# Optimization experiments

Measured on AMD Instinct MI355X. Metric: run time of the kernel, lower is better.

## Reference

```python
import jax, jax.numpy as jnp
import numpy as np
from jax import lax

D_MODEL = 1024
D_STATE = 16
D_CONV = 4
EXPAND = 2
HEADDIM = 64
D_INNER = EXPAND * D_MODEL            # 2048
NHEADS = D_INNER // HEADDIM           # 32
NGROUPS = 1
CONV_DIM = D_INNER + 2 * NGROUPS * D_STATE   # 2080
D_IN_PROJ = 2 * D_INNER + 2 * NGROUPS * D_STATE + NHEADS  # 4160
EPS = 1e-5


def _mamba2(x, in_proj_w, conv_w, conv_b, dt_bias, A_log, Dp, norm_w, out_proj_w):
    # x: (B, L, D_MODEL)
    Bt, L, _ = x.shape
    zxbcdt = jnp.einsum('bld,ed->ble', x, in_proj_w)  # (B,L,D_IN_PROJ)
    z, xBC, dt = jnp.split(zxbcdt, [D_INNER, D_INNER + CONV_DIM], axis=-1)
    dt = jax.nn.softplus(dt + dt_bias)               # (B,L,H)
    # depthwise causal conv over time
    xBC = jnp.swapaxes(xBC, 1, 2)                    # (B,C,L)
    xBC = lax.conv_general_dilated(
        xBC, conv_w, window_strides=(1,), padding=[(D_CONV - 1, 0)],
        feature_group_count=CONV_DIM,
        dimension_numbers=('NCH', 'OIH', 'NCH')) + conv_b[None, :, None]
    xBC = jnp.swapaxes(jax.nn.silu(xBC), 1, 2)       # (B,L,C)
    xs, Bm, Cm = jnp.split(xBC, [D_INNER, D_INNER + D_STATE], axis=-1)
    xs = xs.reshape(Bt, L, NHEADS, HEADDIM)          # (B,L,H,P)
    A = -jnp.exp(A_log)                              # (H,)
    dA = jnp.exp(dt * A)                             # (B,L,H)

    def step(h, inp):
        dA_t, dt_t, B_t, C_t, x_t = inp              # (B,H),(B,H),(B,N),(B,N),(B,H,P)
        h = h * dA_t[:, :, None, None] + jnp.einsum('bh,bn,bhp->bhpn', dt_t, B_t, x_t)
        y = jnp.einsum('bn,bhpn->bhp', C_t, h)
        return h, y

    h0 = jnp.zeros((Bt, NHEADS, HEADDIM, D_STATE), x.dtype)
    xs_seq = (jnp.swapaxes(dA, 0, 1), jnp.swapaxes(dt, 0, 1),
              jnp.swapaxes(Bm, 0, 1), jnp.swapaxes(Cm, 0, 1),
              jnp.swapaxes(xs, 0, 1))
    _, ys = lax.scan(step, h0, xs_seq)               # ys: (L,B,H,P)
    y = jnp.swapaxes(ys, 0, 1) + Dp[None, None, :, None] * xs
    y = y.reshape(Bt, L, D_INNER)
    # gated RMSNorm: gate first (norm_before_gate=False), then rmsnorm
    y = y * jax.nn.silu(z)
    y = y * lax.rsqrt(jnp.mean(y * y, axis=-1, keepdims=True) + EPS) * norm_w
    return jnp.einsum('bld,od->blo', y, out_proj_w)  # (B,L,D_MODEL)


def setup_inputs() -> dict:
    key = jax.random.key(0)
    ks = jax.random.split(key, 20)
    B, L = 2, 2048
    def mamba_params(kidx):
        k = jax.random.split(ks[kidx], 8)
        return dict(
            in_proj_w=jax.random.normal(k[0], (D_IN_PROJ, D_MODEL), jnp.float32) / np.sqrt(D_MODEL),
            conv_w=jax.random.normal(k[1], (CONV_DIM, 1, D_CONV), jnp.float32) / np.sqrt(D_CONV),
            conv_b=jax.random.normal(k[2], (CONV_DIM,), jnp.float32) * 0.01,
            dt_bias=jnp.log(jnp.expm1(jax.random.uniform(k[3], (NHEADS,), jnp.float32, 1e-3, 0.1))),
            A_log=jnp.log(jax.random.uniform(k[4], (NHEADS,), jnp.float32, 1.0, 16.0)),
            Dp=jnp.ones((NHEADS,), jnp.float32),
            norm_w=jnp.ones((D_INNER,), jnp.float32),
            out_proj_w=jax.random.normal(k[5], (D_MODEL, D_INNER), jnp.float32) / np.sqrt(D_INNER),
        )
    pf = mamba_params(1)
    pb = mamba_params(2)
    inp = {'x': jax.random.normal(ks[0], (B, L, D_MODEL), jnp.float32)}
    for name, p in (('fwd', pf), ('bwd', pb)):
        for pk, pv in p.items():
            inp[f'{name}_{pk}'] = pv
    inp['layer_out_proj_w'] = jax.random.normal(ks[3], (D_MODEL, 2 * D_MODEL), jnp.float32) / np.sqrt(2 * D_MODEL)
    inp['layer_scale'] = jnp.full((D_MODEL,), 1e-4, jnp.float32)
    return inp


def reference(x,
              fwd_in_proj_w, fwd_conv_w, fwd_conv_b, fwd_dt_bias, fwd_A_log, fwd_Dp, fwd_norm_w, fwd_out_proj_w,
              bwd_in_proj_w, bwd_conv_w, bwd_conv_b, bwd_dt_bias, bwd_A_log, bwd_Dp, bwd_norm_w, bwd_out_proj_w,
              layer_out_proj_w, layer_scale):
    h_fwd = _mamba2(x, fwd_in_proj_w, fwd_conv_w, fwd_conv_b, fwd_dt_bias, fwd_A_log, fwd_Dp, fwd_norm_w, fwd_out_proj_w)
    x_rev = jnp.flip(x, axis=1)
    h_bwd = jnp.flip(_mamba2(x_rev, bwd_in_proj_w, bwd_conv_w, bwd_conv_b, bwd_dt_bias, bwd_A_log, bwd_Dp, bwd_norm_w, bwd_out_proj_w), axis=1)
    h_bi = jnp.concatenate([h_fwd, h_bwd], axis=-1)   # (B,L,2*D_MODEL)
    mamba_out = jnp.einsum('ble,de->bld', h_bi, layer_out_proj_w)
    # dropout is identity in eval mode
    return x + mamba_out * layer_scale
```

## Files before the change

kernel.cpp:

```cpp
#include <hip/hip_runtime.h>

typedef __attribute__((ext_vector_type(8))) short bf16x8;
typedef __attribute__((ext_vector_type(4))) float f32x4;
typedef __attribute__((ext_vector_type(2))) long i64x2;

#define DEV static __device__ __forceinline__

DEV float b2f(unsigned short u) {
    union { unsigned int u; float f; } c; c.u = ((unsigned int)u) << 16; return c.f;
}
DEV unsigned short f2b(float f) {
    union { float f; unsigned int u; } c; c.f = f;
    unsigned int u = c.u + 0x7fffu + ((c.u >> 16) & 1u);
    return (unsigned short)(u >> 16);
}
DEV float silu_f(float v) { return v / (1.f + __expf(-v)); }

DEV unsigned short cvtpk2(float a, float b) {
    unsigned int d;
    asm("v_cvt_pk_fp8_f32 %0, %1, %2" : "=v"(d) : "v"(a), "v"(b));
    return (unsigned short)d;
}
DEV unsigned char cvt1(float a) { return (unsigned char)cvtpk2(a, 0.f); }

DEV int kperm(int gc) {
    return (gc & ~63) | (((gc >> 3) & 3) << 4) | (((gc >> 5) & 1) << 3) | (gc & 7);
}

#define GLD16(gp, lp) __builtin_amdgcn_global_load_lds( \
    (const __attribute__((address_space(1))) void*)(gp), \
    (__attribute__((address_space(3))) void*)(lp), 16, 0, 0)

#define LSEQ 2048
#define NB 2
#define RTOT 4096
#define DM 1024
#define DI 2048
#define NH 32
#define HP 64
#define NSTATE 16
#define CDIM 2080
#define DIP 4160
#define NW 8320
#define NWP 8448
#define QCH 64
#define NCH (LSEQ / QCH)

struct Cvt8Jobs {
    const float* s0[4];
    const float* s1[4];
    unsigned char* dst[4];
    int rows0[4], rows1[4], rowstot[4], shift[4];
};
__global__ __launch_bounds__(256) void cvt8b_kernel(Cvt8Jobs j) {
    const int jb = blockIdx.y;
    const int gid = blockIdx.x * 256 + threadIdx.x;
    const int shift = j.shift[jb];
    const int tpr = 1 << shift;
    if (gid >= (j.rowstot[jb] << shift)) return;
    const int row = gid >> shift, g = gid & (tpr - 1);
    const int blk = g >> 3, sub = g & 7, lq = sub >> 1, ks = sub & 1;
    const int K = tpr << 3;
    uint2 o;
    const int r0 = j.rows0[jb], r1 = j.rows1[jb];
    if (row < r0 + r1) {
        const float* src = (row < r0 ? j.s0[jb] + (size_t)row * K
                                     : j.s1[jb] + (size_t)(row - r0) * K)
                           + blk * 64 + ks * 32 + lq * 8;
        float4 v0 = *(const float4*)src;
        float4 v1 = *(const float4*)(src + 4);
        o.x = (unsigned)cvtpk2(v0.x, v0.y) | ((unsigned)cvtpk2(v0.z, v0.w) << 16);
        o.y = (unsigned)cvtpk2(v1.x, v1.y) | ((unsigned)cvtpk2(v1.z, v1.w) << 16);
    } else {
        o.x = 0; o.y = 0;
    }
    *(uint2*)(j.dst[jb] + (size_t)row * K + blk * 64 + sub * 8) = o;
}

template<int BM, int BN, int EPI>
__global__ void __launch_bounds__(512, 4)
gemm8_kernel(
    const unsigned char* __restrict__ A0, const unsigned char* __restrict__ B0,
    const unsigned char* __restrict__ A1, const unsigned char* __restrict__ B1,
    void* __restrict__ Cout,
    int Ntot, int K, int ldc, int coff0, int coff1,
    const float* __restrict__ ex, const float* __restrict__ esc)
{
    constexpr int MF = BM / 32;
    constexpr int NI = BN / 64;
    constexpr int GA = BM / 128, GB = BN / 128;
    constexpr int GT = GA + GB;
    constexpr int ABYTES = BM * 64;
    constexpr int BBYTES = BN * 64;
    constexpr int BUFB = ABYTES + BBYTES;
    __shared__ unsigned char lds8[3 * BUFB];

    const unsigned char* __restrict__ A8 = blockIdx.z ? A1 : A0;
    const unsigned char* __restrict__ B8 = blockIdx.z ? B1 : B0;
    const int coff = blockIdx.z ? coff1 : coff0;

    const int nbx = gridDim.x, nby = gridDim.y;
    const int nwg = nbx * nby;
    int id = blockIdx.y * nbx + blockIdx.x;
    {
        const int q = nwg >> 3, r = nwg & 7;
        const int xcd = id & 7, off = id >> 3;
        id = (xcd < r) ? (xcd * (q + 1) + off) : (r * (q + 1) + (xcd - r) * q + off);
    }
    const int gm = 8;
    const int gidx = id / (gm * nbx);
    const int rem  = id - gidx * gm * nbx;
    const int width = min(gm, nby - gidx * gm);
    const int bm = (gidx * gm + rem % width) * BM;
    const int bn = (rem / width) * BN;

    const int tid  = threadIdx.x;
    const int wave = tid >> 6, lane = tid & 63;
    const int wm = wave >> 2, wn = wave & 3;
    const int lr = lane & 15, lq = lane >> 4;
    const int KT = K >> 6;

    int aoff[MF], boff[NI];
#pragma unroll
    for (int mf = 0; mf < MF; ++mf) {
        int row = wm * (BM / 2) + mf * 16 + lr;
        int L = row >> 1, cc = ((row & 1) << 2) | lq;
        aoff[mf] = L * 128 + ((cc ^ (L & 7)) << 4);
    }
#pragma unroll
    for (int ni = 0; ni < NI; ++ni) {
        int row = wn * (BN / 4) + ni * 16 + lr;
        int L = row >> 1, cc = ((row & 1) << 2) | lq;
        boff[ni] = ABYTES + L * 128 + ((cc ^ (L & 7)) << 4);
    }

    auto stage = [&](int ktt, int sbuf) {
#pragma unroll
        for (int q = 0; q < GA; ++q) {
            int u = q * 512 + tid;
            int L = u >> 3, cp = u & 7;
            int cc = cp ^ (L & 7);
            int srow = bm + 2 * L + (cc >> 2);
            const unsigned char* src = A8 + (size_t)srow * K + (ktt << 6) + ((cc & 3) << 4);
            GLD16(src, &lds8[sbuf * BUFB + q * 8192 + ((tid >> 6) << 10)]);
        }
#pragma unroll
        for (int q = 0; q < GB; ++q) {
            int u = q * 512 + tid;
            int L = u >> 3, cp = u & 7;
            int cc = cp ^ (L & 7);
            int srow = bn + 2 * L + (cc >> 2);
            const unsigned char* src = B8 + (size_t)srow * K + (ktt << 6) + ((cc & 3) << 4);
            GLD16(src, &lds8[sbuf * BUFB + ABYTES + q * 8192 + ((tid >> 6) << 10)]);
        }
    };

    f32x4 acc[MF][NI];
#pragma unroll
    for (int i = 0; i < MF; ++i)
#pragma unroll
        for (int j = 0; j < NI; ++j) acc[i][j] = (f32x4){0.f, 0.f, 0.f, 0.f};

    stage(0, 0);
    if (KT > 1) stage(1, 1);
    if constexpr (GT == 3) { asm volatile("s_waitcnt vmcnt(3)" ::: "memory"); }
    else                   { asm volatile("s_waitcnt vmcnt(2)" ::: "memory"); }
    __builtin_amdgcn_sched_barrier(0);
    __builtin_amdgcn_s_barrier();
    __builtin_amdgcn_sched_barrier(0);

    int cur = 0, stg = 2;
    for (int kt = 0; kt < KT; ++kt) {
        const int cb = cur * BUFB;
        const bool dostage = (kt + 2) < KT;
        if (dostage) stage(kt + 2, stg);

        i64x2 av[MF], bv[NI];
#pragma unroll
        for (int mf = 0; mf < MF; ++mf) av[mf] = *(const i64x2*)&lds8[cb + aoff[mf]];
#pragma unroll
        for (int ni = 0; ni < NI; ++ni) bv[ni] = *(const i64x2*)&lds8[cb + boff[ni]];

        __builtin_amdgcn_s_setprio(1);
#pragma unroll
        for (int mf = 0; mf < MF; ++mf)
#pragma unroll
            for (int ni = 0; ni < NI; ++ni) {
                acc[mf][ni] = __builtin_amdgcn_mfma_f32_16x16x32_fp8_fp8(av[mf].x, bv[ni].x, acc[mf][ni], 0, 0, 0);
                acc[mf][ni] = __builtin_amdgcn_mfma_f32_16x16x32_fp8_fp8(av[mf].y, bv[ni].y, acc[mf][ni], 0, 0, 0);
            }
        __builtin_amdgcn_s_setprio(0);

        if (dostage) {
            if constexpr (GT == 3) { asm volatile("s_waitcnt vmcnt(3)" ::: "memory"); }
            else                   { asm volatile("s_waitcnt vmcnt(2)" ::: "memory"); }
        } else {
            asm volatile("s_waitcnt vmcnt(0)" ::: "memory");
        }
        __builtin_amdgcn_sched_barrier(0);
        __builtin_amdgcn_s_barrier();
        __builtin_amdgcn_sched_barrier(0);

        cur = (cur == 2) ? 0 : cur + 1;
        stg = (stg == 2) ? 0 : stg + 1;
    }

#pragma unroll
    for (int mf = 0; mf < MF; ++mf)
#pragma unroll
        for (int ni = 0; ni < NI; ++ni)
#pragma unroll
            for (int r = 0; r < 4; ++r) {
                int grow = bm + wm * (BM / 2) + mf * 16 + lq * 4 + r;
                int gcol = bn + wn * (BN / 4) + ni * 16 + lr;
                float v = acc[mf][ni][r];
                if (EPI == 1) {
                    if (gcol < Ntot)
                        ((unsigned short*)Cout)[(size_t)grow * ldc + coff + gcol] = f2b(v);
                } else if (EPI == 2) {
                    size_t idx = (size_t)grow * ldc + gcol;
                    ((float*)Cout)[idx] = ex[idx] + v * esc[gcol];
                } else {
                    int gc = coff + gcol;
                    ((unsigned char*)Cout)[(size_t)grow * ldc + kperm(gc)] = cvt1(v);
                }
            }
}

#define TCV 32
__global__ __launch_bounds__(256) void conv_kernel(
    const unsigned short* __restrict__ ZX,
    const float* __restrict__ cwF, const float* __restrict__ cbF,
    const float* __restrict__ cwB, const float* __restrict__ cbB,
    const float* __restrict__ dtbiasF, const float* __restrict__ AlogF,
    const float* __restrict__ dtbiasB, const float* __restrict__ AlogB,
    unsigned short* __restrict__ xs,
    float* __restrict__ Bc, float* __restrict__ Cc,
    float* __restrict__ dtb, float* __restrict__ dAb)
{
    const int c = blockIdx.x * 256 + threadIdx.x;
    const int t0 = blockIdx.y * TCV;
    const int db = blockIdx.z;
    const int d = db >> 1, b = db & 1;

    if (c >= CDIM) {
        if (c >= CDIM + NH) return;
        const int h = c - CDIM;
        const float bias = (d ? dtbiasB : dtbiasF)[h];
        const float A = -__expf((d ? AlogB : AlogF)[h]);
        const unsigned short* zp = ZX + (size_t)d * DIP + (DI + CDIM) + h;
#pragma unroll 4
        for (int i = 0; i < TCV; ++i) {
            int t = t0 + i;
            float raw = b2f(zp[((size_t)b * LSEQ + t) * NW]);
            float xv = raw + bias;
            float dtv = (xv > 20.f) ? xv : __logf(1.f + __expf(xv));
            int idx = (db * LSEQ + t) * NH + h;
            dtb[idx] = dtv;
            dAb[idx] = __expf(dtv * A);
        }
        return;
    }

    const float* cw = d ? cwB : cwF;
    const float* cb = d ? cbB : cbF;
    float4 w = *(const float4*)&cw[c * 4];
    const float bias = cb[c];
    const unsigned short* base = ZX + (size_t)d * DIP + DI + c;

    auto ldg = [&](int t) -> float {
        return (t >= 0 && t < LSEQ) ? b2f(base[(size_t)(b * LSEQ + t) * NW]) : 0.f;
    };
    auto emit = [&](int t, float acc) {
        float v = silu_f(acc);
        const int row = b * LSEQ + t;
        if (c < DI) {
            xs[((size_t)d * RTOT + row) * DI + c] = f2b(v);
        } else if (c < DI + NSTATE) {
            Bc[((size_t)db * LSEQ + t) * NSTATE + (c - DI)] = v;
        } else {
            Cc[((size_t)db * LSEQ + t) * NSTATE + (c - DI - NSTATE)] = v;
        }
    };

    if (d == 0) {
        float v0 = ldg(t0 - 3), v1 = ldg(t0 - 2), v2 = ldg(t0 - 1), vt = ldg(t0);
#pragma unroll 4
        for (int i = 0; i < TCV; ++i) {
            float vn = (i < TCV - 1) ? ldg(t0 + i + 1) : 0.f;
            emit(t0 + i, bias + w.x * v0 + w.y * v1 + w.z * v2 + w.w * vt);
            v0 = v1; v1 = v2; v2 = vt; vt = vn;
        }
    } else {
        float v3 = ldg(t0 + TCV + 2), v2 = ldg(t0 + TCV + 1), v1 = ldg(t0 + TCV), vt = ldg(t0 + TCV - 1);
#pragma unroll 4
        for (int i = TCV - 1; i >= 0; --i) {
            float vn = (i > 0) ? ldg(t0 + i - 1) : 0.f;
            emit(t0 + i, bias + w.w * vt + w.z * v1 + w.y * v2 + w.x * v3);
            v3 = v2; v2 = v1; v1 = vt; vt = vn;
        }
    }
}

#define LD16V(dst, ptr) do { const float4* _p = (const float4*)(ptr); \
    float4 _q0 = _p[0], _q1 = _p[1], _q2 = _p[2], _q3 = _p[3]; \
    dst[0]=_q0.x; dst[1]=_q0.y; dst[2]=_q0.z; dst[3]=_q0.w; \
    dst[4]=_q1.x; dst[5]=_q1.y; dst[6]=_q1.z; dst[7]=_q1.w; \
    dst[8]=_q2.x; dst[9]=_q2.y; dst[10]=_q2.z; dst[11]=_q2.w; \
    dst[12]=_q3.x; dst[13]=_q3.y; dst[14]=_q3.z; dst[15]=_q3.w; } while (0)

#define ST16V(ptr, src) do { float4* _p = (float4*)(ptr); \
    _p[0] = make_float4(src[0],src[1],src[2],src[3]); \
    _p[1] = make_float4(src[4],src[5],src[6],src[7]); \
    _p[2] = make_float4(src[8],src[9],src[10],src[11]); \
    _p[3] = make_float4(src[12],src[13],src[14],src[15]); } while (0)

__global__ __launch_bounds__(64) void chunk_state_kernel(
    const unsigned short* __restrict__ xs,
    const float* __restrict__ Bc,
    const float* __restrict__ dtb, const float* __restrict__ dAb,
    float* __restrict__ Sbuf,
    float* __restrict__ Pbuf)
{
    const int h = blockIdx.x, db = blockIdx.y, c = blockIdx.z;
    const int d = db >> 1, b = db & 1;
    const int lane = threadIdx.x;
    float hs[16];
#pragma unroll
    for (int n = 0; n < 16; ++n) hs[n] = 0.f;
    float pacc = 1.f;
    const size_t dbase = (size_t)d * RTOT;
    const int s0 = c * QCH;

    float xq0, xq1, xq2, xq3, dtq0, dtq1, dtq2, dtq3, dAq0, dAq1, dAq2, dAq3;
    float BA[16], BB[16];

#define SIDX(ii) (d ? (LSEQ - 1 - (s0 + min((ii), QCH - 1))) : (s0 + min((ii), QCH - 1)))
#define XL(S, ii) do { const int _t = SIDX(ii); \
    const size_t _row = (size_t)b * LSEQ + _t, _rdb = (size_t)db * LSEQ + _t; \
    xq##S = b2f(xs[(dbase + _row) * DI + h * HP + lane]); \
    dtq##S = dtb[_rdb * 32 + h]; dAq##S = dAb[_rdb * 32 + h]; } while (0)
#define BL(BUF, ii) do { const int _t = SIDX(ii); \
    const size_t _rdb = (size_t)db * LSEQ + _t; LD16V(BUF, Bc + _rdb * 16); } while (0)
#define SC(S, BUF) do { const float _dtx = dtq##S * xq##S; \
    _Pragma("unroll") for (int n = 0; n < 16; ++n) hs[n] = fmaf(hs[n], dAq##S, BUF[n] * _dtx); \
    pacc *= dAq##S; } while (0)

    XL(0, 0); XL(1, 1); XL(2, 2);
    BL(BA, 0);
    for (int ii = 0; ii < QCH; ii += 4) {
        XL(3, ii + 3); BL(BB, ii + 1); SC(0, BA);
        XL(0, ii + 4); BL(BA, ii + 2); SC(1, BB);
        XL(1, ii + 5); BL(BB, ii + 3); SC(2, BA);
        XL(2, ii + 6); BL(BA, ii + 4); SC(3, BB);
    }
#undef SIDX
#undef XL
#undef BL
#undef SC

    float* Sp = Sbuf + (((size_t)(db * NH + h)) * NCH + c) * 1024 + lane * 16;
    ST16V(Sp, hs);
    if (lane == 0) Pbuf[(db * NH + h) * NCH + c] = pacc;
}

__global__ __launch_bounds__(64) void chunk_combine_kernel(
    const float* __restrict__ Sbuf, const float* __restrict__ Pbuf,
    float* __restrict__ Hbuf)
{
    const int idx = blockIdx.x;
    const int lane = threadIdx.x;
    float hs[16];
#pragma unroll
    for (int n = 0; n < 16; ++n) hs[n] = 0.f;
    float* H0 = Hbuf + ((size_t)idx * NCH) * 1024 + lane * 16;
    ST16V(H0, hs);
    for (int c = 0; c < NCH - 1; ++c) {
        const float* Sp = Sbuf + ((size_t)idx * NCH + c) * 1024 + lane * 16;
        float S[16];
        LD16V(S, Sp);
        const float P = Pbuf[idx * NCH + c];
#pragma unroll
        for (int n = 0; n < 16; ++n) hs[n] = fmaf(hs[n], P, S[n]);
        float* Hp = Hbuf + ((size_t)idx * NCH + c + 1) * 1024 + lane * 16;
        ST16V(Hp, hs);
    }
}

__global__ __launch_bounds__(64) void chunk_scan_kernel(
    const unsigned short* __restrict__ xs,
    const float* __restrict__ Bc, const float* __restrict__ Cc,
    const float* __restrict__ dtb, const float* __restrict__ dAb,
    const float* __restrict__ DpF, const float* __restrict__ DpB,
    const float* __restrict__ Hbuf,
    unsigned short* __restrict__ ybuf)
{
    const int h = blockIdx.x, db = blockIdx.y, c = blockIdx.z;
    const int d = db >> 1, b = db & 1;
    const int lane = threadIdx.x;
    const float Dp = (d ? DpB : DpF)[h];
    float hs[16];
    {
        const float* Hp = Hbuf + ((size_t)(db * NH + h) * NCH + c) * 1024 + lane * 16;
        LD16V(hs, Hp);
    }
    const size_t dbase = (size_t)d * RTOT;
    const int s0 = c * QCH;

    float xq0, xq1, xq2, xq3, dtq0, dtq1, dtq2, dtq3, dAq0, dAq1, dAq2, dAq3;
    float BA[16], BB[16], CA[16], CB[16];

#define SIDX(ii) (d ? (LSEQ - 1 - (s0 + min((ii), QCH - 1))) : (s0 + min((ii), QCH - 1)))
#define XL(S, ii) do { const int _t = SIDX(ii); \
    const size_t _row = (size_t)b * LSEQ + _t, _rdb = (size_t)db * LSEQ + _t; \
    xq##S = b2f(xs[(dbase + _row) * DI + h * HP + lane]); \
    dtq##S = dtb[_rdb * 32 + h]; dAq##S = dAb[_rdb * 32 + h]; } while (0)
#define BLC(BUF, CBUF, ii) do { const int _t = SIDX(ii); \
    const size_t _rdb = (size_t)db * LSEQ + _t; \
    LD16V(BUF, Bc + _rdb * 16); LD16V(CBUF, Cc + _rdb * 16); } while (0)
#define SCY(S, BUF, CBUF, iv) do { const float _dtx = dtq##S * xq##S; \
    float _y0 = 0.f, _y1 = 0.f, _y2 = 0.f, _y3 = 0.f; \
    _Pragma("unroll") for (int n = 0; n < 16; n += 4) { \
        hs[n]   = fmaf(hs[n],   dAq##S, BUF[n]   * _dtx); _y0 = fmaf(CBUF[n],   hs[n],   _y0); \
        hs[n+1] = fmaf(hs[n+1], dAq##S, BUF[n+1] * _dtx); _y1 = fmaf(CBUF[n+1], hs[n+1], _y1); \
        hs[n+2] = fmaf(hs[n+2], dAq##S, BUF[n+2] * _dtx); _y2 = fmaf(CBUF[n+2], hs[n+2], _y2); \
        hs[n+3] = fmaf(hs[n+3], dAq##S, BUF[n+3] * _dtx); _y3 = fmaf(CBUF[n+3], hs[n+3], _y3); } \
    const int _t = d ? (LSEQ - 1 - (s0 + (iv))) : (s0 + (iv)); \
    const size_t _row = (size_t)b * LSEQ + _t; \
    ybuf[(dbase + _row) * DI + h * HP + lane] = f2b(((_y0 + _y1) + (_y2 + _y3)) + Dp * xq##S); } while (0)

    XL(0, 0); XL(1, 1); XL(2, 2);
    BLC(BA, CA, 0);
    for (int ii = 0; ii < QCH; ii += 4) {
        XL(3, ii + 3); BLC(BB, CB, ii + 1); SCY(0, BA, CA, ii);
        XL(0, ii + 4); BLC(BA, CA, ii + 2); SCY(1, BB, CB, ii + 1);
        XL(1, ii + 5); BLC(BB, CB, ii + 3); SCY(2, BA, CA, ii + 2);
        XL(2, ii + 6); BLC(BA, CA, ii + 4); SCY(3, BB, CB, ii + 3);
    }
#undef SIDX
#undef XL
#undef BLC
#undef SCY
}

__global__ __launch_bounds__(256) void gatenorm_kernel(
    const unsigned short* __restrict__ ybuf, const unsigned short* __restrict__ ZX,
    const float* __restrict__ nwF, const float* __restrict__ nwB,
    unsigned char* __restrict__ yg8)
{
    const int r = blockIdx.x;
    const int d = blockIdx.y;
    const int tid = threadIdx.x;
    const float* nw = d ? nwB : nwF;
    const int c0 = tid * 8;
    const unsigned short* yp = ybuf + ((size_t)d * RTOT + r) * DI + c0;
    const unsigned short* zp = ZX + (size_t)r * NW + d * DIP + c0;
    uint4 yv = *(const uint4*)yp;
    uint4 zv = *(const uint4*)zp;
    unsigned int yw[4] = {yv.x, yv.y, yv.z, yv.w};
    unsigned int zw[4] = {zv.x, zv.y, zv.z, zv.w};
    float g[8]; float ss = 0.f;
#pragma unroll
    for (int i = 0; i < 8; ++i) {
        unsigned short yu = (i & 1) ? (unsigned short)(yw[i >> 1] >> 16) : (unsigned short)(yw[i >> 1] & 0xffff);
        unsigned short zu = (i & 1) ? (unsigned short)(zw[i >> 1] >> 16) : (unsigned short)(zw[i >> 1] & 0xffff);
        float y = b2f(yu), z = b2f(zu);
        float gv = y * silu_f(z);
        g[i] = gv; ss += gv * gv;
    }
#pragma unroll
    for (int m = 1; m < 64; m <<= 1) ss += __shfl_xor(ss, m, 64);
    __shared__ float red[4];
    if ((tid & 63) == 0) red[tid >> 6] = ss;
    __syncthreads();
    float tot = red[0] + red[1] + red[2] + red[3];
    float sc = rsqrtf(tot * (1.f / 2048.f) + 1e-5f);
    uint2 o;
    o.x = (unsigned)cvtpk2(g[0] * sc * nw[c0 + 0], g[1] * sc * nw[c0 + 1])
        | ((unsigned)cvtpk2(g[2] * sc * nw[c0 + 2], g[3] * sc * nw[c0 + 3]) << 16);
    o.y = (unsigned)cvtpk2(g[4] * sc * nw[c0 + 4], g[5] * sc * nw[c0 + 5])
        | ((unsigned)cvtpk2(g[6] * sc * nw[c0 + 6], g[7] * sc * nw[c0 + 7]) << 16);
    const int pos = (c0 & ~63) | (((c0 >> 3) & 3) << 4) | (((c0 >> 5) & 1) << 3);
    *(uint2*)(yg8 + ((size_t)d * RTOT + r) * DI + pos) = o;
}

extern "C" void kernel_launch(void* const* d_in, const int* in_sizes, int n_in,
                              void* d_out, int out_size, void* d_ws, size_t ws_size,
                              hipStream_t stream)
{
    const float* x     = (const float*)d_in[0];
    const float* fin   = (const float*)d_in[1];
    const float* fcw   = (const float*)d_in[2];
    const float* fcb   = (const float*)d_in[3];
    const float* fdtb  = (const float*)d_in[4];
    const float* fAlog = (const float*)d_in[5];
    const float* fDp   = (const float*)d_in[6];
    const float* fnw   = (const float*)d_in[7];
    const float* fout  = (const float*)d_in[8];
    const float* bin   = (const float*)d_in[9];
    const float* bcw   = (const float*)d_in[10];
    const float* bcb   = (const float*)d_in[11];
    const float* bdtb  = (const float*)d_in[12];
    const float* bAlog = (const float*)d_in[13];
    const float* bDp   = (const float*)d_in[14];
    const float* bnw   = (const float*)d_in[15];
    const float* bout  = (const float*)d_in[16];
    const float* lw    = (const float*)d_in[17];
    const float* lsc   = (const float*)d_in[18];

    char* w = (char*)d_ws;
    auto alloc = [&](size_t bytes) { char* p = w; w += (bytes + 255) & ~(size_t)255; return p; };
    unsigned char*  xb8  = (unsigned char*)alloc((size_t)RTOT * DM);
    unsigned char*  win8 = (unsigned char*)alloc((size_t)NWP * DM);
    unsigned char*  wo8  = (unsigned char*)alloc((size_t)2 * DM * DI);
    unsigned char*  wl8  = (unsigned char*)alloc((size_t)DM * DI);
    unsigned short* zx  = (unsigned short*)alloc((size_t)RTOT * NW * 2);
    unsigned short* xs  = (unsigned short*)alloc((size_t)2 * RTOT * DI * 2);
    float* Bc  = (float*)alloc((size_t)2 * RTOT * NSTATE * 4);
    float* Cc  = (float*)alloc((size_t)2 * RTOT * NSTATE * 4);
    float* dtb = (float*)alloc((size_t)2 * RTOT * NH * 4);
    float* dAb = (float*)alloc((size_t)2 * RTOT * NH * 4);
    unsigned short* yb  = (unsigned short*)alloc((size_t)2 * RTOT * DI * 2);
    unsigned char*  yg8 = (unsigned char*)alloc((size_t)2 * RTOT * DI);
    unsigned char*  hbi8= (unsigned char*)alloc((size_t)RTOT * DI);
    float* Pbuf = (float*)alloc((size_t)128 * NCH * 4);
    float* Sbuf = (float*)alloc((size_t)128 * NCH * 1024 * 4);
    float* Hbuf = (float*)alloc((size_t)128 * NCH * 1024 * 4);
    (void)ws_size; (void)in_sizes; (void)n_in; (void)out_size;

    Cvt8Jobs j;
    j.s0[0] = x;    j.s1[0] = x;    j.dst[0] = xb8;  j.rows0[0] = RTOT; j.rows1[0] = 0;    j.rowstot[0] = RTOT; j.shift[0] = 7;
    j.s0[1] = fin;  j.s1[1] = bin;  j.dst[1] = win8; j.rows0[1] = DIP;  j.rows1[1] = DIP;  j.rowstot[1] = NWP;  j.shift[1] = 7;
    j.s0[2] = fout; j.s1[2] = bout; j.dst[2] = wo8;  j.rows0[2] = DM;   j.rows1[2] = DM;   j.rowstot[2] = 2 * DM; j.shift[2] = 8;
    j.s0[3] = lw;   j.s1[3] = lw;   j.dst[3] = wl8;  j.rows0[3] = DM;   j.rows1[3] = 0;    j.rowstot[3] = DM;   j.shift[3] = 8;
    cvt8b_kernel<<<dim3((NWP * 128 + 255) / 256, 4), 256, 0, stream>>>(j);

    gemm8_kernel<128, 256, 1><<<dim3(NWP / 256, RTOT / 128), 512, 0, stream>>>(
        xb8, win8, nullptr, nullptr, zx, NW, DM, NW, 0, 0, nullptr, nullptr);

    conv_kernel<<<dim3((CDIM + NH + 255) / 256, LSEQ / TCV, 4), 256, 0, stream>>>(
        zx, fcw, fcb, bcw, bcb, fdtb, fAlog, bdtb, bAlog, xs, Bc, Cc, dtb, dAb);

    chunk_state_kernel<<<dim3(NH, 4, NCH - 1), 64, 0, stream>>>(
        xs, Bc, dtb, dAb, Sbuf, Pbuf);
    chunk_combine_kernel<<<128, 64, 0, stream>>>(Sbuf, Pbuf, Hbuf);
    chunk_scan_kernel<<<dim3(NH, 4, NCH), 64, 0, stream>>>(
        xs, Bc, Cc, dtb, dAb, fDp, bDp, Hbuf, yb);

    gatenorm_kernel<<<dim3(RTOT, 2), 256, 0, stream>>>(yb, zx, fnw, bnw, yg8);

    gemm8_kernel<128, 256, 3><<<dim3(DM / 256, RTOT / 128, 2), 512, 0, stream>>>(
        yg8, wo8, yg8 + (size_t)RTOT * DI, wo8 + (size_t)DM * DI,
        hbi8, DM, DI, DI, 0, DM, nullptr, nullptr);

    gemm8_kernel<128, 128, 2><<<dim3(DM / 128, RTOT / 128), 512, 0, stream>>>(
        hbi8, wl8, nullptr, nullptr, d_out, DM, DI, DM, 0, 0, x, lsc);
}
```

Measured before the change: 297.3 us.

## Deepen FP8 GEMM pipeline to four LDS stages and shrink N tiles

The FP8 GEMM kernel moves from a three-buffer to a four-buffer LDS ring, prefetching three k-tiles ahead with vmcnt waits scaled to the number of loads per stage. It also skips the barrier after the final iteration. The in-projection and per-direction out-projection GEMMs switch from 128x256 to 128x128 tiles, which doubles their grid size for better CU occupancy. The cost is more LDS per block, which may limit blocks per CU, and smaller tiles that reuse each loaded operand less.

```diff
diff --git a/kernel.cpp b/kernel.cpp
--- a/kernel.cpp
+++ b/kernel.cpp
@@ -86,14 +86,16 @@
     int Ntot, int K, int ldc, int coff0, int coff1,
     const float* __restrict__ ex, const float* __restrict__ esc)
 {
+    constexpr int NT = 512;
     constexpr int MF = BM / 32;
     constexpr int NI = BN / 64;
-    constexpr int GA = BM / 128, GB = BN / 128;
-    constexpr int GT = GA + GB;
     constexpr int ABYTES = BM * 64;
     constexpr int BBYTES = BN * 64;
     constexpr int BUFB = ABYTES + BBYTES;
-    __shared__ unsigned char lds8[3 * BUFB];
+    constexpr int QA = ABYTES / (NT * 16);
+    constexpr int QB = BBYTES / (NT * 16);
+    constexpr int GT = QA + QB;
+    __shared__ unsigned char lds8[4 * BUFB];
 
     const unsigned char* __restrict__ A8 = blockIdx.z ? A1 : A0;
     const unsigned char* __restrict__ B8 = blockIdx.z ? B1 : B0;
@@ -136,22 +138,22 @@
 
     auto stage = [&](int ktt, int sbuf) {
 #pragma unroll
-        for (int q = 0; q < GA; ++q) {
-            int u = q * 512 + tid;
+        for (int q = 0; q < QA; ++q) {
+            int u = q * NT + tid;
             int L = u >> 3, cp = u & 7;
             int cc = cp ^ (L & 7);
             int srow = bm + 2 * L + (cc >> 2);
             const unsigned char* src = A8 + (size_t)srow * K + (ktt << 6) + ((cc & 3) << 4);
-            GLD16(src, &lds8[sbuf * BUFB + q * 8192 + ((tid >> 6) << 10)]);
-        }
-#pragma unroll
-        for (int q = 0; q < GB; ++q) {
-            int u = q * 512 + tid;
+            GLD16(src, &lds8[sbuf * BUFB + q * (NT * 16) + (wave << 10)]);
+        }
+#pragma unroll
+        for (int q = 0; q < QB; ++q) {
+            int u = q * NT + tid;
             int L = u >> 3, cp = u & 7;
             int cc = cp ^ (L & 7);
             int srow = bn + 2 * L + (cc >> 2);
             const unsigned char* src = B8 + (size_t)srow * K + (ktt << 6) + ((cc & 3) << 4);
-            GLD16(src, &lds8[sbuf * BUFB + ABYTES + q * 8192 + ((tid >> 6) << 10)]);
+            GLD16(src, &lds8[sbuf * BUFB + ABYTES + q * (NT * 16) + (wave << 10)]);
         }
     };
 
@@ -163,17 +165,17 @@
 
     stage(0, 0);
     if (KT > 1) stage(1, 1);
-    if constexpr (GT == 3) { asm volatile("s_waitcnt vmcnt(3)" ::: "memory"); }
-    else                   { asm volatile("s_waitcnt vmcnt(2)" ::: "memory"); }
+    if (KT > 2) stage(2, 2);
+    if (KT > 2)      { asm volatile("s_waitcnt vmcnt(%0)" :: "n"(2 * GT) : "memory"); }
+    else if (KT > 1) { asm volatile("s_waitcnt vmcnt(%0)" :: "n"(GT) : "memory"); }
+    else             { asm volatile("s_waitcnt vmcnt(0)" ::: "memory"); }
     __builtin_amdgcn_sched_barrier(0);
     __builtin_amdgcn_s_barrier();
     __builtin_amdgcn_sched_barrier(0);
 
-    int cur = 0, stg = 2;
     for (int kt = 0; kt < KT; ++kt) {
-        const int cb = cur * BUFB;
-        const bool dostage = (kt + 2) < KT;
-        if (dostage) stage(kt + 2, stg);
+        const int cb = (kt & 3) * BUFB;
+        if (kt + 3 < KT) stage(kt + 3, (kt + 3) & 3);
 
         i64x2 av[MF], bv[NI];
 #pragma unroll
@@ -191,18 +193,14 @@
             }
         __builtin_amdgcn_s_setprio(0);
 
-        if (dostage) {
-            if constexpr (GT == 3) { asm volatile("s_waitcnt vmcnt(3)" ::: "memory"); }
-            else                   { asm volatile("s_waitcnt vmcnt(2)" ::: "memory"); }
-        } else {
-            asm volatile("s_waitcnt vmcnt(0)" ::: "memory");
-        }
-        __builtin_amdgcn_sched_barrier(0);
-        __builtin_amdgcn_s_barrier();
-        __builtin_amdgcn_sched_barrier(0);
-
-        cur = (cur == 2) ? 0 : cur + 1;
-        stg = (stg == 2) ? 0 : stg + 1;
+        if (kt + 1 < KT) {
+            if (kt + 3 < KT)      { asm volatile("s_waitcnt vmcnt(%0)" :: "n"(2 * GT) : "memory"); }
+            else if (kt + 2 < KT) { asm volatile("s_waitcnt vmcnt(%0)" :: "n"(GT) : "memory"); }
+            else                  { asm volatile("s_waitcnt vmcnt(0)" ::: "memory"); }
+            __builtin_amdgcn_sched_barrier(0);
+            __builtin_amdgcn_s_barrier();
+            __builtin_amdgcn_sched_barrier(0);
+        }
     }
 
 #pragma unroll
@@ -535,7 +533,7 @@
     j.s0[3] = lw;   j.s1[3] = lw;   j.dst[3] = wl8;  j.rows0[3] = DM;   j.rows1[3] = 0;    j.rowstot[3] = DM;   j.shift[3] = 8;
     cvt8b_kernel<<<dim3((NWP * 128 + 255) / 256, 4), 256, 0, stream>>>(j);
 
-    gemm8_kernel<128, 256, 1><<<dim3(NWP / 256, RTOT / 128), 512, 0, stream>>>(
+    gemm8_kernel<128, 128, 1><<<dim3(NWP / 128, RTOT / 128), 512, 0, stream>>>(
         xb8, win8, nullptr, nullptr, zx, NW, DM, NW, 0, 0, nullptr, nullptr);
 
     conv_kernel<<<dim3((CDIM + NH + 255) / 256, LSEQ / TCV, 4), 256, 0, stream>>>(
@@ -549,7 +547,7 @@
 
     gatenorm_kernel<<<dim3(RTOT, 2), 256, 0, stream>>>(yb, zx, fnw, bnw, yg8);
 
-    gemm8_kernel<128, 256, 3><<<dim3(DM / 256, RTOT / 128, 2), 512, 0, stream>>>(
+    gemm8_kernel<128, 128, 3><<<dim3(DM / 128, RTOT / 128, 2), 512, 0, stream>>>(
         yg8, wo8, yg8 + (size_t)RTOT * DI, wo8 + (size_t)DM * DI,
         hbi8, DM, DI, DI, 0, DM, nullptr, nullptr);
 
```

Measured after the change: 296.5 us. No clear change (-0.3%).
